# Kernel tuning notes

Hardware: AMD Instinct MI355X
Metric: run time of the kernel (lower is better)

## Reference

```python
import jax, jax.numpy as jnp
import numpy as np

H = 500      # hidden size of RNNCell
D_IN = 512   # VGG16 feature channels
D_OUT = 100  # output vocab/logit dim
STEPS = 49   # 7x7 spatial grid consumed sequentially


def setup_inputs() -> dict:
    key = jax.random.key(0)
    ks = jax.random.split(key, 8)
    # post-VGG16 feature map for one 224x224 image: [1, 512, 7, 7]
    x = jax.random.normal(ks[0], (1, D_IN, 7, 7), dtype=jnp.float32)
    # original code uses torch.rand for the initial hidden state
    hidden0 = jax.random.uniform(ks[1], (1, H), dtype=jnp.float32)
    # nn.RNNCell(512, 500) params, PyTorch layout: W_ih [H, D_IN], W_hh [H, H]
    s_rnn = 1.0 / np.sqrt(H)
    W_ih = jax.random.uniform(ks[2], (H, D_IN), minval=-s_rnn, maxval=s_rnn, dtype=jnp.float32)
    W_hh = jax.random.uniform(ks[3], (H, H), minval=-s_rnn, maxval=s_rnn, dtype=jnp.float32)
    b_ih = jax.random.uniform(ks[4], (H,), minval=-s_rnn, maxval=s_rnn, dtype=jnp.float32)
    b_hh = jax.random.uniform(ks[5], (H,), minval=-s_rnn, maxval=s_rnn, dtype=jnp.float32)
    # nn.Linear(500, 100): W_out [D_OUT, H]
    s_out = 1.0 / np.sqrt(H)
    W_out = jax.random.uniform(ks[6], (D_OUT, H), minval=-s_out, maxval=s_out, dtype=jnp.float32)
    b_out = jax.random.uniform(ks[7], (D_OUT,), minval=-s_out, maxval=s_out, dtype=jnp.float32)
    return {"x": x, "hidden0": hidden0, "W_ih": W_ih, "W_hh": W_hh,
            "b_ih": b_ih, "b_hh": b_hh, "W_out": W_out, "b_out": b_out}


def reference(x, hidden0, W_ih, W_hh, b_ih, b_hh, W_out, b_out):
    # x: [1, 512, 7, 7] -> permute(0,2,3,1) -> [1,7,7,512] -> view(49, 1, 512)
    seq = jnp.transpose(x, (0, 2, 3, 1)).reshape(STEPS, 1, D_IN)
    # Precompute the input projection for all steps in one GEMM: [49, 1, H]
    xproj = jnp.einsum('tbd,hd->tbh', seq, W_ih) + b_ih + b_hh

    def step(h, xp):
        # h: [1, H]; RNNCell: h' = tanh(x W_ih^T + b_ih + h W_hh^T + b_hh)
        h = jnp.tanh(xp + h @ W_hh.T)
        out = jnp.tanh(h @ W_out.T + b_out)  # [1, D_OUT]
        return h, out

    _, outs = jax.lax.scan(step, hidden0, xproj)  # outs: [49, 1, 100]
    # torch.stack(op, 0).squeeze().unsqueeze(0) -> [1, 49, 100]
    return outs.squeeze(1)[None, :, :]
```

## Files before the change

### kernel.cpp

```cpp
#include <hip/hip_runtime.h>
#include <hip/hip_bf16.h>

#define H 500
#define D_IN 512
#define D_OUT 100
#define STEPS 49

typedef _Float16 h2_t __attribute__((ext_vector_type(2)));

#if defined(__has_builtin)
#if __has_builtin(__builtin_amdgcn_fdot2)
#define HAVE_FDOT2 1
#endif
#endif

__device__ __forceinline__ float fdot2f(h2_t a, h2_t b, float c) {
#ifdef HAVE_FDOT2
    return __builtin_amdgcn_fdot2(a, b, c, false);
#else
    return c + (float)a[0] * (float)b[0] + (float)a[1] * (float)b[1];
#endif
}
__device__ __forceinline__ h2_t bch2(unsigned u) { return __builtin_bit_cast(h2_t, u); }

__global__ void k0_pack(const float* __restrict__ W_hh,
                        uint4* __restrict__ blobW, uint2* __restrict__ blobW2,
                        uint4* __restrict__ blobTA, uint2* __restrict__ blobTB) {
    const int T = blockIdx.x * 256 + threadIdx.x;
    const int k = T >> 9, tid = T & 511;
    const int w = tid >> 6, l = tid & 63;
    const int row = l + 64 * k;
    const int c0 = w * 64;

    _Float16 v[64];
    if (row < H && w < 7) {
        const float4* src = (const float4*)(W_hh + row * H + c0);
#pragma unroll
        for (int q = 0; q < 16; q++) {
            const float4 f = src[q];
            v[4 * q + 0] = (_Float16)f.x; v[4 * q + 1] = (_Float16)f.y;
            v[4 * q + 2] = (_Float16)f.z; v[4 * q + 3] = (_Float16)f.w;
        }
    } else {
#pragma unroll
        for (int i = 0; i < 64; i++) {
            const int c = c0 + i;
            v[i] = (row < H && c < H) ? (_Float16)W_hh[row * H + c] : (_Float16)0.f;
        }
    }
    unsigned up[32];
#pragma unroll
    for (int i = 0; i < 32; i++) {
        h2_t p{v[2 * i], v[2 * i + 1]};
        up[i] = __builtin_bit_cast(unsigned, p);
    }
#pragma unroll
    for (int j4 = 0; j4 < 6; j4++) {
        uint4 u; u.x = up[4*j4]; u.y = up[4*j4+1]; u.z = up[4*j4+2]; u.w = up[4*j4+3];
        blobW[(k * 6 + j4) * 512 + tid] = u;
    }
    { uint2 u; u.x = up[24]; u.y = up[25]; blobW2[k * 512 + tid] = u; }
    { uint4 u; u.x = up[26]; u.y = up[27]; u.z = up[28]; u.w = up[29]; blobTA[k * 512 + tid] = u; }
    { uint2 u; u.x = up[30]; u.y = up[31]; blobTB[k * 512 + tid] = u; }
}

__global__ void k1_xproj(const float* __restrict__ x, const float* __restrict__ W_ih,
                         const float* __restrict__ b_ih, const float* __restrict__ b_hh,
                         float* __restrict__ xproj) {
    const int r = blockIdx.x;
    const int lane = threadIdx.x;
    float w[8];
#pragma unroll
    for (int k = 0; k < 8; k++) w[k] = W_ih[r * D_IN + k * 64 + lane];
    float p[STEPS];
#pragma unroll
    for (int t = 0; t < STEPS; t++) p[t] = 0.f;
#pragma unroll
    for (int k = 0; k < 8; k++) {
        const float* xr = x + (size_t)(k * 64 + lane) * STEPS;
#pragma unroll
        for (int t = 0; t < STEPS; t++) p[t] = fmaf(w[k], xr[t], p[t]);
    }
#pragma unroll
    for (int t = 0; t < STEPS; t++) {
        float v = p[t];
        v += __shfl_xor(v, 32); v += __shfl_xor(v, 16); v += __shfl_xor(v, 8);
        v += __shfl_xor(v, 4);  v += __shfl_xor(v, 2);  v += __shfl_xor(v, 1);
        p[t] = v;
    }
    if (lane == 0) {
        const float b = b_ih[r] + b_hh[r];
        for (int t = 0; t < STEPS; t++) xproj[t * H + r] = p[t] + b;
    }
}

__global__ __attribute__((amdgpu_flat_work_group_size(512, 512)))
__attribute__((amdgpu_waves_per_eu(2, 2)))
void k2_scan(const float* __restrict__ hidden0,
             const uint4* __restrict__ blobW, const uint2* __restrict__ blobW2,
             const uint4* __restrict__ blobTA, const uint2* __restrict__ blobTB,
             const float* __restrict__ xproj, float* __restrict__ Hs) {
    __shared__ uint4 WlA[8][512];
    __shared__ uint2 WlB[8][512];
    __shared__ float pbuf[8][512];
    __shared__ __align__(16) _Float16 h16[512];

    const int tid = threadIdx.x, w = tid >> 6, l = tid & 63;

    h2_t wreg[8][26];
#pragma unroll
    for (int k = 0; k < 8; k++) {
#pragma unroll
        for (int j4 = 0; j4 < 6; j4++) {
            const uint4 u = blobW[(k * 6 + j4) * 512 + tid];
            wreg[k][4 * j4 + 0] = bch2(u.x);
            wreg[k][4 * j4 + 1] = bch2(u.y);
            wreg[k][4 * j4 + 2] = bch2(u.z);
            wreg[k][4 * j4 + 3] = bch2(u.w);
        }
        const uint2 u2 = blobW2[k * 512 + tid];
        wreg[k][24] = bch2(u2.x);
        wreg[k][25] = bch2(u2.y);
        WlA[w][l + 64 * k] = blobTA[k * 512 + tid];
        WlB[w][l + 64 * k] = blobTB[k * 512 + tid];
    }
    h16[tid] = (tid < H) ? (_Float16)hidden0[tid] : (_Float16)0.f;
    __syncthreads();

    const int rs = (tid < H) ? tid : 0;
    for (int t = 0; t < STEPS; t++) {
        const float xp = xproj[t * H + rs];

        float a[8] = {0.f, 0.f, 0.f, 0.f, 0.f, 0.f, 0.f, 0.f};
        const uint4* hsl = (const uint4*)(h16 + w * 64);
#pragma unroll
        for (int b = 0; b < 6; b++) {
            const uint4 hb = hsl[b];
            const h2_t hp0 = bch2(hb.x), hp1 = bch2(hb.y),
                       hp2 = bch2(hb.z), hp3 = bch2(hb.w);
#pragma unroll
            for (int k = 0; k < 8; k++) {
                a[k] = fdot2f(wreg[k][4 * b + 0], hp0, a[k]);
                a[k] = fdot2f(wreg[k][4 * b + 1], hp1, a[k]);
                a[k] = fdot2f(wreg[k][4 * b + 2], hp2, a[k]);
                a[k] = fdot2f(wreg[k][4 * b + 3], hp3, a[k]);
            }
        }
        const uint4 hb6 = hsl[6];
        const uint4 hb7 = hsl[7];
        const h2_t hp24 = bch2(hb6.x), hp25 = bch2(hb6.y);
        const h2_t hpA0 = bch2(hb6.z), hpA1 = bch2(hb6.w);
        const h2_t hpA2 = bch2(hb7.x), hpA3 = bch2(hb7.y);
        const h2_t hpB0 = bch2(hb7.z), hpB1 = bch2(hb7.w);
#pragma unroll
        for (int k = 0; k < 8; k++) {
            const int r = l + 64 * k;
            const uint4 ta = WlA[w][r];
            const uint2 tb = WlB[w][r];
            a[k] = fdot2f(wreg[k][24], hp24, a[k]);
            a[k] = fdot2f(wreg[k][25], hp25, a[k]);
            a[k] = fdot2f(bch2(ta.x), hpA0, a[k]);
            a[k] = fdot2f(bch2(ta.y), hpA1, a[k]);
            a[k] = fdot2f(bch2(ta.z), hpA2, a[k]);
            a[k] = fdot2f(bch2(ta.w), hpA3, a[k]);
            a[k] = fdot2f(bch2(tb.x), hpB0, a[k]);
            a[k] = fdot2f(bch2(tb.y), hpB1, a[k]);
        }
#pragma unroll
        for (int k = 0; k < 8; k++) pbuf[w][64 * k + l] = a[k];
        __syncthreads();

        float s = 0.f;
#pragma unroll
        for (int w2 = 0; w2 < 8; w2++) s += pbuf[w2][tid];
        const float hval = tanhf(s + xp);
        if (tid < H) Hs[t * 512 + tid] = hval;
        h16[tid] = (tid < H) ? (_Float16)hval : (_Float16)0.f;
        __syncthreads();
    }
}

__global__ void k3_out(const float* __restrict__ Hs, const float* __restrict__ W_out,
                       const float* __restrict__ b_out, float* __restrict__ out) {
    const int t = blockIdx.x, o = threadIdx.x;
    if (o < D_OUT) {
        const float4* wr = (const float4*)(W_out + o * H);
        const float4* hr = (const float4*)(Hs + t * 512);
        float acc = b_out[o];
#pragma unroll 5
        for (int i = 0; i < 125; i++) {
            const float4 wv = wr[i];
            const float4 hv = hr[i];
            acc = fmaf(wv.x, hv.x, acc);
            acc = fmaf(wv.y, hv.y, acc);
            acc = fmaf(wv.z, hv.z, acc);
            acc = fmaf(wv.w, hv.w, acc);
        }
        out[t * D_OUT + o] = tanhf(acc);
    }
}

extern "C" void kernel_launch(void* const* d_in, const int* in_sizes, int n_in,
                              void* d_out, int out_size, void* d_ws, size_t ws_size,
                              hipStream_t stream) {
    const float* x       = (const float*)d_in[0];
    const float* hidden0 = (const float*)d_in[1];
    const float* W_ih    = (const float*)d_in[2];
    const float* W_hh    = (const float*)d_in[3];
    const float* b_ih    = (const float*)d_in[4];
    const float* b_hh    = (const float*)d_in[5];
    const float* W_out   = (const float*)d_in[6];
    const float* b_out   = (const float*)d_in[7];
    float* out = (float*)d_out;

    char* ws = (char*)d_ws;
    uint4* blobW  = (uint4*)(ws);
    uint2* blobW2 = (uint2*)(ws + 393216);
    uint4* blobTA = (uint4*)(ws + 425984);
    uint2* blobTB = (uint2*)(ws + 491520);
    float* xproj  = (float*)(ws + 524288);
    float* Hs     = (float*)(ws);

    k0_pack<<<16, 256, 0, stream>>>(W_hh, blobW, blobW2, blobTA, blobTB);
    k1_xproj<<<H, 64, 0, stream>>>(x, W_ih, b_ih, b_hh, xproj);
    k2_scan<<<1, 512, 0, stream>>>(hidden0, blobW, blobW2, blobTA, blobTB, xproj, Hs);
    k3_out<<<STEPS, 128, 0, stream>>>(Hs, W_out, b_out, out);
}
```

Measured before the change: 106.1 us.

## Fuse pack and xproj kernels, shrink register weights, use fast tanh

The W_hh packing and input-projection kernels are merged into one launch of 141 blocks, with the xproj part now running four rows per 256-thread block, which removes one kernel launch. In the scan kernel, each thread keeps 24 instead of 26 packed half2 weights in registers, with asm pins to stop rematerialisation. The remaining 16 columns per wave move to two uint4 shared-memory tiles instead of a uint4 plus a uint2. tanhf is replaced by an exp-based fast tanh in both the scan and output kernels, which shortens the serial per-step critical path but may lose accuracy near zero or overflow for large inputs.

```diff
diff --git a/kernel.cpp b/kernel.cpp
--- a/kernel.cpp
+++ b/kernel.cpp
@@ -23,104 +23,107 @@
 }
 __device__ __forceinline__ h2_t bch2(unsigned u) { return __builtin_bit_cast(h2_t, u); }
 
-__global__ void k0_pack(const float* __restrict__ W_hh,
-                        uint4* __restrict__ blobW, uint2* __restrict__ blobW2,
-                        uint4* __restrict__ blobTA, uint2* __restrict__ blobTB) {
-    const int T = blockIdx.x * 256 + threadIdx.x;
-    const int k = T >> 9, tid = T & 511;
-    const int w = tid >> 6, l = tid & 63;
-    const int row = l + 64 * k;
-    const int c0 = w * 64;
-
-    _Float16 v[64];
-    if (row < H && w < 7) {
-        const float4* src = (const float4*)(W_hh + row * H + c0);
-#pragma unroll
-        for (int q = 0; q < 16; q++) {
-            const float4 f = src[q];
-            v[4 * q + 0] = (_Float16)f.x; v[4 * q + 1] = (_Float16)f.y;
-            v[4 * q + 2] = (_Float16)f.z; v[4 * q + 3] = (_Float16)f.w;
-        }
+__device__ __forceinline__ float tanh_fast(float x) {
+    const float e = __expf(2.f * x);
+    return 1.f - 2.f / (e + 1.f);
+}
+
+#define PINV(x) asm volatile("" : "+v"(x))
+
+__global__ void k01_pack_xproj(const float* __restrict__ W_hh, const float* __restrict__ x,
+                               const float* __restrict__ W_ih, const float* __restrict__ b_ih,
+                               const float* __restrict__ b_hh,
+                               uint4* __restrict__ blobW, uint4* __restrict__ blobTA,
+                               uint4* __restrict__ blobTB, float* __restrict__ xproj) {
+    if (blockIdx.x < 16) {
+        const int T = blockIdx.x * 256 + threadIdx.x;
+        const int k = T >> 9, tid = T & 511;
+        const int w = tid >> 6, l = tid & 63;
+        const int row = l + 64 * k;
+        const int c0 = w * 64;
+
+        _Float16 v[64];
+        if (row < H && w < 7) {
+            const float4* src = (const float4*)(W_hh + row * H + c0);
+#pragma unroll
+            for (int q = 0; q < 16; q++) {
+                const float4 f = src[q];
+                v[4 * q + 0] = (_Float16)f.x; v[4 * q + 1] = (_Float16)f.y;
+                v[4 * q + 2] = (_Float16)f.z; v[4 * q + 3] = (_Float16)f.w;
+            }
+        } else {
+#pragma unroll
+            for (int i = 0; i < 64; i++) {
+                const int c = c0 + i;
+                v[i] = (row < H && c < H) ? (_Float16)W_hh[row * H + c] : (_Float16)0.f;
+            }
+        }
+        unsigned up[32];
+#pragma unroll
+        for (int i = 0; i < 32; i++) {
+            h2_t p{v[2 * i], v[2 * i + 1]};
+            up[i] = __builtin_bit_cast(unsigned, p);
+        }
+#pragma unroll
+        for (int j4 = 0; j4 < 6; j4++) {
+            uint4 u; u.x = up[4*j4]; u.y = up[4*j4+1]; u.z = up[4*j4+2]; u.w = up[4*j4+3];
+            blobW[(k * 6 + j4) * 512 + tid] = u;
+        }
+        { uint4 u; u.x = up[24]; u.y = up[25]; u.z = up[26]; u.w = up[27]; blobTA[k * 512 + tid] = u; }
+        { uint4 u; u.x = up[28]; u.y = up[29]; u.z = up[30]; u.w = up[31]; blobTB[k * 512 + tid] = u; }
     } else {
-#pragma unroll
-        for (int i = 0; i < 64; i++) {
-            const int c = c0 + i;
-            v[i] = (row < H && c < H) ? (_Float16)W_hh[row * H + c] : (_Float16)0.f;
-        }
-    }
-    unsigned up[32];
-#pragma unroll
-    for (int i = 0; i < 32; i++) {
-        h2_t p{v[2 * i], v[2 * i + 1]};
-        up[i] = __builtin_bit_cast(unsigned, p);
-    }
-#pragma unroll
-    for (int j4 = 0; j4 < 6; j4++) {
-        uint4 u; u.x = up[4*j4]; u.y = up[4*j4+1]; u.z = up[4*j4+2]; u.w = up[4*j4+3];
-        blobW[(k * 6 + j4) * 512 + tid] = u;
-    }
-    { uint2 u; u.x = up[24]; u.y = up[25]; blobW2[k * 512 + tid] = u; }
-    { uint4 u; u.x = up[26]; u.y = up[27]; u.z = up[28]; u.w = up[29]; blobTA[k * 512 + tid] = u; }
-    { uint2 u; u.x = up[30]; u.y = up[31]; blobTB[k * 512 + tid] = u; }
-}
-
-__global__ void k1_xproj(const float* __restrict__ x, const float* __restrict__ W_ih,
-                         const float* __restrict__ b_ih, const float* __restrict__ b_hh,
-                         float* __restrict__ xproj) {
-    const int r = blockIdx.x;
-    const int lane = threadIdx.x;
-    float w[8];
-#pragma unroll
-    for (int k = 0; k < 8; k++) w[k] = W_ih[r * D_IN + k * 64 + lane];
-    float p[STEPS];
-#pragma unroll
-    for (int t = 0; t < STEPS; t++) p[t] = 0.f;
-#pragma unroll
-    for (int k = 0; k < 8; k++) {
-        const float* xr = x + (size_t)(k * 64 + lane) * STEPS;
-#pragma unroll
-        for (int t = 0; t < STEPS; t++) p[t] = fmaf(w[k], xr[t], p[t]);
-    }
-#pragma unroll
-    for (int t = 0; t < STEPS; t++) {
-        float v = p[t];
-        v += __shfl_xor(v, 32); v += __shfl_xor(v, 16); v += __shfl_xor(v, 8);
-        v += __shfl_xor(v, 4);  v += __shfl_xor(v, 2);  v += __shfl_xor(v, 1);
-        p[t] = v;
-    }
-    if (lane == 0) {
-        const float b = b_ih[r] + b_hh[r];
-        for (int t = 0; t < STEPS; t++) xproj[t * H + r] = p[t] + b;
-    }
-}
-
-__global__ __attribute__((amdgpu_flat_work_group_size(512, 512)))
-__attribute__((amdgpu_waves_per_eu(2, 2)))
-void k2_scan(const float* __restrict__ hidden0,
-             const uint4* __restrict__ blobW, const uint2* __restrict__ blobW2,
-             const uint4* __restrict__ blobTA, const uint2* __restrict__ blobTB,
-             const float* __restrict__ xproj, float* __restrict__ Hs) {
+        const int wv = threadIdx.x >> 6, lane = threadIdx.x & 63;
+        const int r = (blockIdx.x - 16) * 4 + wv;
+        if (r >= H) return;
+        float wr[8];
+#pragma unroll
+        for (int k = 0; k < 8; k++) wr[k] = W_ih[r * D_IN + k * 64 + lane];
+        float p[STEPS];
+#pragma unroll
+        for (int t = 0; t < STEPS; t++) p[t] = 0.f;
+#pragma unroll
+        for (int k = 0; k < 8; k++) {
+            const float* xr = x + (size_t)(k * 64 + lane) * STEPS;
+#pragma unroll
+            for (int t = 0; t < STEPS; t++) p[t] = fmaf(wr[k], xr[t], p[t]);
+        }
+#pragma unroll
+        for (int t = 0; t < STEPS; t++) {
+            float v = p[t];
+            v += __shfl_xor(v, 32); v += __shfl_xor(v, 16); v += __shfl_xor(v, 8);
+            v += __shfl_xor(v, 4);  v += __shfl_xor(v, 2);  v += __shfl_xor(v, 1);
+            p[t] = v;
+        }
+        if (lane == 0) {
+            const float b = b_ih[r] + b_hh[r];
+            for (int t = 0; t < STEPS; t++) xproj[t * H + r] = p[t] + b;
+        }
+    }
+}
+
+__global__ void __launch_bounds__(512, 2)
+k2_scan(const float* __restrict__ hidden0,
+        const uint4* __restrict__ blobW, const uint4* __restrict__ blobTA,
+        const uint4* __restrict__ blobTB,
+        const float* __restrict__ xproj, float* __restrict__ Hs) {
     __shared__ uint4 WlA[8][512];
-    __shared__ uint2 WlB[8][512];
+    __shared__ uint4 WlB[8][512];
     __shared__ float pbuf[8][512];
     __shared__ __align__(16) _Float16 h16[512];
 
     const int tid = threadIdx.x, w = tid >> 6, l = tid & 63;
 
-    h2_t wreg[8][26];
+    unsigned wreg[8][24];
 #pragma unroll
     for (int k = 0; k < 8; k++) {
 #pragma unroll
         for (int j4 = 0; j4 < 6; j4++) {
             const uint4 u = blobW[(k * 6 + j4) * 512 + tid];
-            wreg[k][4 * j4 + 0] = bch2(u.x);
-            wreg[k][4 * j4 + 1] = bch2(u.y);
-            wreg[k][4 * j4 + 2] = bch2(u.z);
-            wreg[k][4 * j4 + 3] = bch2(u.w);
-        }
-        const uint2 u2 = blobW2[k * 512 + tid];
-        wreg[k][24] = bch2(u2.x);
-        wreg[k][25] = bch2(u2.y);
+            wreg[k][4 * j4 + 0] = u.x; PINV(wreg[k][4 * j4 + 0]);
+            wreg[k][4 * j4 + 1] = u.y; PINV(wreg[k][4 * j4 + 1]);
+            wreg[k][4 * j4 + 2] = u.z; PINV(wreg[k][4 * j4 + 2]);
+            wreg[k][4 * j4 + 3] = u.w; PINV(wreg[k][4 * j4 + 3]);
+        }
         WlA[w][l + 64 * k] = blobTA[k * 512 + tid];
         WlB[w][l + 64 * k] = blobTB[k * 512 + tid];
     }
@@ -140,31 +143,31 @@
                        hp2 = bch2(hb.z), hp3 = bch2(hb.w);
 #pragma unroll
             for (int k = 0; k < 8; k++) {
-                a[k] = fdot2f(wreg[k][4 * b + 0], hp0, a[k]);
-                a[k] = fdot2f(wreg[k][4 * b + 1], hp1, a[k]);
-                a[k] = fdot2f(wreg[k][4 * b + 2], hp2, a[k]);
-                a[k] = fdot2f(wreg[k][4 * b + 3], hp3, a[k]);
+                a[k] = fdot2f(bch2(wreg[k][4 * b + 0]), hp0, a[k]);
+                a[k] = fdot2f(bch2(wreg[k][4 * b + 1]), hp1, a[k]);
+                a[k] = fdot2f(bch2(wreg[k][4 * b + 2]), hp2, a[k]);
+                a[k] = fdot2f(bch2(wreg[k][4 * b + 3]), hp3, a[k]);
             }
         }
         const uint4 hb6 = hsl[6];
         const uint4 hb7 = hsl[7];
-        const h2_t hp24 = bch2(hb6.x), hp25 = bch2(hb6.y);
-        const h2_t hpA0 = bch2(hb6.z), hpA1 = bch2(hb6.w);
-        const h2_t hpA2 = bch2(hb7.x), hpA3 = bch2(hb7.y);
-        const h2_t hpB0 = bch2(hb7.z), hpB1 = bch2(hb7.w);
+        const h2_t hpA0 = bch2(hb6.x), hpA1 = bch2(hb6.y),
+                   hpA2 = bch2(hb6.z), hpA3 = bch2(hb6.w);
+        const h2_t hpB0 = bch2(hb7.x), hpB1 = bch2(hb7.y),
+                   hpB2 = bch2(hb7.z), hpB3 = bch2(hb7.w);
 #pragma unroll
         for (int k = 0; k < 8; k++) {
             const int r = l + 64 * k;
             const uint4 ta = WlA[w][r];
-            const uint2 tb = WlB[w][r];
-            a[k] = fdot2f(wreg[k][24], hp24, a[k]);
-            a[k] = fdot2f(wreg[k][25], hp25, a[k]);
+            const uint4 tb = WlB[w][r];
             a[k] = fdot2f(bch2(ta.x), hpA0, a[k]);
             a[k] = fdot2f(bch2(ta.y), hpA1, a[k]);
             a[k] = fdot2f(bch2(ta.z), hpA2, a[k]);
             a[k] = fdot2f(bch2(ta.w), hpA3, a[k]);
             a[k] = fdot2f(bch2(tb.x), hpB0, a[k]);
             a[k] = fdot2f(bch2(tb.y), hpB1, a[k]);
+            a[k] = fdot2f(bch2(tb.z), hpB2, a[k]);
+            a[k] = fdot2f(bch2(tb.w), hpB3, a[k]);
         }
 #pragma unroll
         for (int k = 0; k < 8; k++) pbuf[w][64 * k + l] = a[k];
@@ -173,7 +176,7 @@
         float s = 0.f;
 #pragma unroll
         for (int w2 = 0; w2 < 8; w2++) s += pbuf[w2][tid];
-        const float hval = tanhf(s + xp);
+        const float hval = tanh_fast(s + xp);
         if (tid < H) Hs[t * 512 + tid] = hval;
         h16[tid] = (tid < H) ? (_Float16)hval : (_Float16)0.f;
         __syncthreads();
@@ -196,7 +199,7 @@
             acc = fmaf(wv.z, hv.z, acc);
             acc = fmaf(wv.w, hv.w, acc);
         }
-        out[t * D_OUT + o] = tanhf(acc);
+        out[t * D_OUT + o] = tanh_fast(acc);
     }
 }
 
@@ -215,14 +218,13 @@
 
     char* ws = (char*)d_ws;
     uint4* blobW  = (uint4*)(ws);
-    uint2* blobW2 = (uint2*)(ws + 393216);
-    uint4* blobTA = (uint4*)(ws + 425984);
-    uint2* blobTB = (uint2*)(ws + 491520);
+    uint4* blobTA = (uint4*)(ws + 393216);
+    uint4* blobTB = (uint4*)(ws + 458752);
     float* xproj  = (float*)(ws + 524288);
     float* Hs     = (float*)(ws);
 
-    k0_pack<<<16, 256, 0, stream>>>(W_hh, blobW, blobW2, blobTA, blobTB);
-    k1_xproj<<<H, 64, 0, stream>>>(x, W_ih, b_ih, b_hh, xproj);
-    k2_scan<<<1, 512, 0, stream>>>(hidden0, blobW, blobW2, blobTA, blobTB, xproj, Hs);
+    k01_pack_xproj<<<141, 256, 0, stream>>>(W_hh, x, W_ih, b_ih, b_hh,
+                                            blobW, blobTA, blobTB, xproj);
+    k2_scan<<<1, 512, 0, stream>>>(hidden0, blobW, blobTA, blobTB, xproj, Hs);
     k3_out<<<STEPS, 128, 0, stream>>>(Hs, W_out, b_out, out);
 }
```

Measured after the change: 108.2 us. About the same (+2.0%).
